# Performance work log

Measured on AMD Instinct MI355X. Metric: run time of the kernel, lower is better.

## Reference

```python
import jax, jax.numpy as jnp
import numpy as np

K = 32
TEMP = 0.01
OTHERWEIGHT = 0.5
BS = 64
F = 128


def setup_inputs() -> dict:
    key = jax.random.key(0)
    k1, k2, k3 = jax.random.split(key, 3)
    feats1 = jax.random.normal(k1, (K * BS, F), dtype=jnp.float32)
    feats2 = jax.random.normal(k2, (K * BS, F), dtype=jnp.float32)
    overlap_inds = jax.random.randint(k3, (K,), 0, 2).astype(bool)
    return {"feats1": feats1, "feats2": feats2, "overlap_inds": overlap_inds, "bs": BS}


def _labels(overlap_inds, bs):
    k = overlap_inds.shape[0]
    labels1 = jnp.repeat(jnp.arange(k), bs)
    nov = (~overlap_inds).astype(jnp.int32)
    excl_nov = jnp.cumsum(nov) - nov  # exclusive count of non-overlaps before i
    class2 = jnp.where(overlap_inds, jnp.arange(k), k + excl_nov)
    labels2 = jnp.repeat(class2, bs)
    return jnp.concatenate([labels1, labels2])


def reference(feats1, feats2, overlap_inds, bs):
    n1 = feats1.shape[0]
    labels = _labels(overlap_inds, bs)            # [n]
    feats = jnp.concatenate([feats1, feats2])     # [n, F]
    n = feats.shape[0]

    logits = (feats @ feats.T) * TEMP             # [n, n]; log of exp(sim*temp)
    sim = jnp.exp(logits)

    same = labels[:, None] == labels[None, :]
    eye = jnp.eye(n, dtype=bool)
    pos_mask = same & ~eye
    neg_mask = ~same

    is2 = jnp.arange(n) >= n1                     # second-view block indicator
    cross_w = jnp.where(is2[:, None] != is2[None, :], OTHERWEIGHT, 1.0)

    neg_sum = jnp.sum(jnp.where(neg_mask, sim, 0.0), axis=1)      # [n]
    # -log(pos / neg_sum) = log(neg_sum) - logits
    per_pair_loss = cross_w * (jnp.log(neg_sum)[:, None] - logits)
    total_loss = jnp.sum(jnp.where(pos_mask, per_pair_loss, 0.0))
    total_pos = jnp.sum(pos_mask)

    # accuracy: a positive pair counts iff its sim beats ALL negatives in its row
    max_neg = jnp.max(jnp.where(neg_mask, sim, -jnp.inf), axis=1)  # [n]
    correct = pos_mask & (sim > max_neg[:, None])
    acc = jnp.sum(correct).astype(jnp.float32) / total_pos.astype(jnp.float32)

    loss = total_loss / total_pos.astype(jnp.float32)
    return acc, loss
```

## Files before the change

kernel.cpp:

```cpp
#include <hip/hip_runtime.h>
#include <math.h>

#define TEMP 0.01f

typedef __attribute__((ext_vector_type(8))) short short8;
typedef __attribute__((ext_vector_type(4))) float f32x4;
typedef __attribute__((ext_vector_type(8))) unsigned short ushort8_t;


__device__ __forceinline__ unsigned bf16_hi_bits(float x) {
  unsigned u = __float_as_uint(x);
  return (u + 0x7FFFu + ((u >> 16) & 1u)) >> 16;
}

struct HL { unsigned short h, l; };

__device__ __forceinline__ HL split1(float x) {
  unsigned hb = bf16_hi_bits(x);
  float hf = __uint_as_float(hb << 16);
  unsigned lb = bf16_hi_bits(x - hf);
  HL r;
  r.h = (unsigned short)hb;
  r.l = (unsigned short)lb;
  return r;
}

__device__ __forceinline__ void decode_ov(const int* __restrict__ ov_raw,
                                          int* s_class2, int* s_v2b,
                                          int* s_ov) {
  const int t = threadIdx.x;
  if (t < 64) {
    int v = (t < 32) ? ov_raw[t] : 0;
    bool valid = (t >= 32) || (v == 0) || (v == 1);
    unsigned long long okmask = __ballot(valid);
    bool as_int = (okmask == ~0ull);
    s_v2b[t] = 0;
    if (t < 32) {
      int o = as_int ? v : (((const unsigned char*)ov_raw)[t] ? 1 : 0);
      s_ov[t] = o;
      unsigned long long nz = __ballot((t < 32) && !o);
      int cum = __popcll(nz & ((1ull << t) - 1ull));
      int c2 = o ? t : 32 + cum;
      s_class2[t] = c2;
      s_v2b[c2] = t;
    }
  }
}

__device__ __forceinline__ int labf(int g, const int* s_class2) {
  return (g < 2048) ? (g >> 6) : s_class2[(g - 2048) >> 6];
}

__device__ __forceinline__ int slotf(int g, int cls, const int* s_v2b) {
  if (g < 2048) return g - (cls << 6);
  return ((cls < 32) ? 64 : 0) + (g - 2048 - (s_v2b[cls] << 6));
}

__global__ __launch_bounds__(256) void precompute_kernel(
    const float* __restrict__ f1, const float* __restrict__ f2,
    unsigned short* __restrict__ Ph, unsigned short* __restrict__ Pl) {
  const int u = blockIdx.x * 256 + threadIdx.x;
  const int row = u >> 4;
  const int gid = u & 15;
  const int kc = gid >> 3, P = gid & 7;
  const int k = kc * 64 + (P ^ (row & 7)) * 8;
  const float* src = (row < 2048) ? (f1 + (size_t)row * 128)
                                  : (f2 + (size_t)(row - 2048) * 128);
  const float4 a = *(const float4*)(src + k);
  const float4 b = *(const float4*)(src + k + 4);
  ushort8_t hi, lo;
  HL s;
  s = split1(a.x); hi.s0 = s.h; lo.s0 = s.l;
  s = split1(a.y); hi.s1 = s.h; lo.s1 = s.l;
  s = split1(a.z); hi.s2 = s.h; lo.s2 = s.l;
  s = split1(a.w); hi.s3 = s.h; lo.s3 = s.l;
  s = split1(b.x); hi.s4 = s.h; lo.s4 = s.l;
  s = split1(b.y); hi.s5 = s.h; lo.s5 = s.l;
  s = split1(b.z); hi.s6 = s.h; lo.s6 = s.l;
  s = split1(b.w); hi.s7 = s.h; lo.s7 = s.l;
  *(ushort8_t*)&Ph[(size_t)row * 128 + gid * 8] = hi;
  *(ushort8_t*)&Pl[(size_t)row * 128 + gid * 8] = lo;
}

__device__ __forceinline__ void compute_tile(
    int ibase, int jbase, bool diag,
    const unsigned short* __restrict__ Ph, const unsigned short* __restrict__ Pl,
    unsigned short (*Ah)[64], unsigned short (*Al)[64],
    unsigned short (*Bh)[64], unsigned short (*Bl)[64],
    const int* s_class2, const int* s_v2b,
    float* __restrict__ nsum, int* __restrict__ nmaxb,
    float* __restrict__ pcw, float* __restrict__ pcwl,
    float* __restrict__ posbuf) {
  const int t = threadIdx.x;
  const int l = t & 63;
  const int wid = t >> 6;
  const int wy = wid >> 1, wx = wid & 1;
  const int rr = l & 15;
  const int q = l >> 4;
  const int sw = l & 7;

  f32x4 acc[4][4];
#pragma unroll
  for (int mi = 0; mi < 4; ++mi)
#pragma unroll
    for (int ni = 0; ni < 4; ++ni) acc[mi][ni] = (f32x4)0.0f;

  const int gg = t & 7;
  const int r0 = t >> 3;

  for (int kc = 0; kc < 2; ++kc) {
    __syncthreads();
#pragma unroll
    for (int p = 0; p < 4; ++p) {
      const int r = r0 + 32 * p;
      const size_t arec = (size_t)(ibase + r) * 128 + kc * 64 + gg * 8;
      const ushort8_t vah = *(const ushort8_t*)&Ph[arec];
      const ushort8_t val = *(const ushort8_t*)&Pl[arec];
      *(ushort8_t*)&Ah[r][gg * 8] = vah;
      *(ushort8_t*)&Al[r][gg * 8] = val;
      if (!diag) {
        const size_t brec = (size_t)(jbase + r) * 128 + kc * 64 + gg * 8;
        const ushort8_t vbh = *(const ushort8_t*)&Ph[brec];
        const ushort8_t vbl = *(const ushort8_t*)&Pl[brec];
        *(ushort8_t*)&Bh[r][gg * 8] = vbh;
        *(ushort8_t*)&Bl[r][gg * 8] = vbl;
      }
    }
    __syncthreads();

#pragma unroll
    for (int s = 0; s < 2; ++s) {
      const int pb = ((((s << 2) | q)) ^ sw) << 3;
      short8 afh[4], afl[4], bfh[4], bfl[4];
#pragma unroll
      for (int mi = 0; mi < 4; ++mi) {
        const int ar = wy * 64 + mi * 16 + rr;
        afh[mi] = *(const short8*)&Ah[ar][pb];
        afl[mi] = *(const short8*)&Al[ar][pb];
        const int br = wx * 64 + mi * 16 + rr;
        bfh[mi] = diag ? *(const short8*)&Ah[br][pb]
                       : *(const short8*)&Bh[br][pb];
        bfl[mi] = diag ? *(const short8*)&Al[br][pb]
                       : *(const short8*)&Bl[br][pb];
      }
#pragma unroll
      for (int mi = 0; mi < 4; ++mi)
#pragma unroll
        for (int ni = 0; ni < 4; ++ni) {
          acc[mi][ni] = __builtin_amdgcn_mfma_f32_16x16x32_bf16(
              afh[mi], bfh[ni], acc[mi][ni], 0, 0, 0);
          acc[mi][ni] = __builtin_amdgcn_mfma_f32_16x16x32_bf16(
              afh[mi], bfl[ni], acc[mi][ni], 0, 0, 0);
          acc[mi][ni] = __builtin_amdgcn_mfma_f32_16x16x32_bf16(
              afl[mi], bfh[ni], acc[mi][ni], 0, 0, 0);
        }
    }
  }

  const bool off = !diag;
  const float cw = ((ibase < 2048) != (jbase < 2048)) ? 0.5f : 1.0f;
  int gj[4], lj[4];
#pragma unroll
  for (int ni = 0; ni < 4; ++ni) {
    gj[ni] = jbase + wx * 64 + ni * 16 + rr;
    lj[ni] = labf(gj[ni], s_class2);
  }

  float cnsum[4], cnmax[4], cpcw[4], cpcwl[4];
#pragma unroll
  for (int ni = 0; ni < 4; ++ni) {
    cnsum[ni] = 0.f; cnmax[ni] = 0.f; cpcw[ni] = 0.f; cpcwl[ni] = 0.f;
  }

#pragma unroll
  for (int mi = 0; mi < 4; ++mi) {
#pragma unroll
    for (int reg = 0; reg < 4; ++reg) {
      const int gi = ibase + wy * 64 + mi * 16 + q * 4 + reg;
      const int li = labf(gi, s_class2);
      float rnsum = 0.f, rnmax = 0.f, rpcw = 0.f, rpcwl = 0.f;
#pragma unroll
      for (int ni = 0; ni < 4; ++ni) {
        const int gjj = gj[ni];
        if (gi == gjj) continue;
        const float logit = acc[mi][ni][reg] * TEMP;
        const float e = __expf(logit);
        if (li == lj[ni]) {
          rpcw += cw;
          rpcwl += cw * logit;
          posbuf[(size_t)gi * 128 + slotf(gjj, li, s_v2b)] = e;
          if (off) {
            cpcw[ni] += cw;
            cpcwl[ni] += cw * logit;
            posbuf[(size_t)gjj * 128 + slotf(gi, li, s_v2b)] = e;
          }
        } else {
          rnsum += e;
          rnmax = fmaxf(rnmax, e);
          if (off) {
            cnsum[ni] += e;
            cnmax[ni] = fmaxf(cnmax[ni], e);
          }
        }
      }
#pragma unroll
      for (int m = 1; m < 16; m <<= 1) {
        rnsum += __shfl_xor(rnsum, m, 64);
        rpcw  += __shfl_xor(rpcw, m, 64);
        rpcwl += __shfl_xor(rpcwl, m, 64);
        rnmax = fmaxf(rnmax, __shfl_xor(rnmax, m, 64));
      }
      if (rr == 0) {
        atomicAdd(&nsum[gi], rnsum);
        atomicAdd(&pcw[gi], rpcw);
        atomicAdd(&pcwl[gi], rpcwl);
        atomicMax(&nmaxb[gi], __float_as_int(rnmax));
      }
    }
  }

  if (off) {
#pragma unroll
    for (int ni = 0; ni < 4; ++ni) {
      float cs = cnsum[ni], cm = cnmax[ni], cp = cpcw[ni], cl = cpcwl[ni];
#pragma unroll
      for (int m = 16; m < 64; m <<= 1) {
        cs += __shfl_xor(cs, m, 64);
        cp += __shfl_xor(cp, m, 64);
        cl += __shfl_xor(cl, m, 64);
        cm = fmaxf(cm, __shfl_xor(cm, m, 64));
      }
      if (q == 0) {
        const int g = gj[ni];
        atomicAdd(&nsum[g], cs);
        atomicAdd(&pcw[g], cp);
        atomicAdd(&pcwl[g], cl);
        atomicMax(&nmaxb[g], __float_as_int(cm));
      }
    }
  }
}

__global__ __launch_bounds__(256, 2) void main_kernel(
    const unsigned short* __restrict__ Ph, const unsigned short* __restrict__ Pl,
    const int* __restrict__ ov_raw, float* __restrict__ nsum,
    int* __restrict__ nmaxb, float* __restrict__ pcw,
    float* __restrict__ pcwl, float* __restrict__ posbuf) {
  __shared__ unsigned short Ah[128][64], Al[128][64];
  __shared__ unsigned short Bh[128][64], Bl[128][64];
  __shared__ int s_class2[32], s_v2b[64], s_ov[32];

  decode_ov(ov_raw, s_class2, s_v2b, s_ov);

  const int bid = blockIdx.x;
  if (bid < 496) {
    int idx = bid, bi = 0;
    while (idx >= 31 - bi) { idx -= 31 - bi; ++bi; }
    const int bj = bi + 1 + idx;
    compute_tile(bi * 128, bj * 128, false, Ph, Pl, Ah, Al, Bh, Bl, s_class2,
                 s_v2b, nsum, nmaxb, pcw, pcwl, posbuf);
  } else {
    const int d = (bid - 496) * 2;
    compute_tile(d * 128, d * 128, true, Ph, Pl, Ah, Al, Bh, Bl, s_class2,
                 s_v2b, nsum, nmaxb, pcw, pcwl, posbuf);
    compute_tile((d + 1) * 128, (d + 1) * 128, true, Ph, Pl, Ah, Al, Bh, Bl,
                 s_class2, s_v2b, nsum, nmaxb, pcw, pcwl, posbuf);
  }
}

__global__ __launch_bounds__(256) void finalize_kernel(
    const int* __restrict__ ov_raw, const float* __restrict__ nsum,
    const int* __restrict__ nmaxb, const float* __restrict__ pcw,
    const float* __restrict__ pcwl, const float* __restrict__ posbuf,
    float* __restrict__ accum, int* __restrict__ counter,
    float* __restrict__ out) {
  __shared__ int s_class2[32], s_v2b[64], s_ov[32];
  __shared__ float sc[4], sp[4], sl[4];
  decode_ov(ov_raw, s_class2, s_v2b, s_ov);
  __syncthreads();

  const int t = threadIdx.x;
  const int w = t >> 6, lane = t & 63;
  float cnt_acc = 0.f, pos_acc = 0.f, loss_acc = 0.f;
  const int rbase = blockIdx.x * 64 + w * 16;
  for (int i = 0; i < 16; ++i) {
    const int row = rbase + i;
    const float2 pv = *(const float2*)&posbuf[(size_t)row * 128 + lane * 2];
    const int c = labf(row, s_class2);
    const int size = (c < 32) ? (s_ov[c] ? 128 : 64) : 64;
    int selfslot;
    if (row < 2048) selfslot = row - (c << 6);
    else selfslot = ((c < 32) ? 64 : 0) + (row - 2048 - (s_v2b[c] << 6));
    const float nmax = __int_as_float(nmaxb[row]);
    const int s0 = lane * 2;
    int h = 0;
    if (s0 < size && s0 != selfslot && pv.x > nmax) h++;
    if (s0 + 1 < size && s0 + 1 != selfslot && pv.y > nmax) h++;
    cnt_acc += (float)h;
    if (lane == 0) {
      loss_acc += logf(nsum[row]) * pcw[row] - pcwl[row];
      pos_acc += (float)(size - 1);
    }
  }
#pragma unroll
  for (int m = 1; m < 64; m <<= 1) {
    cnt_acc += __shfl_xor(cnt_acc, m, 64);
    pos_acc += __shfl_xor(pos_acc, m, 64);
    loss_acc += __shfl_xor(loss_acc, m, 64);
  }
  if (lane == 0) { sc[w] = cnt_acc; sp[w] = pos_acc; sl[w] = loss_acc; }
  __syncthreads();
  if (t == 0) {
    atomicAdd(&accum[0], sc[0] + sc[1] + sc[2] + sc[3]);
    atomicAdd(&accum[1], sp[0] + sp[1] + sp[2] + sp[3]);
    atomicAdd(&accum[2], sl[0] + sl[1] + sl[2] + sl[3]);
    __threadfence();
    const int prev = atomicAdd(counter, 1);
    if (prev == 63) {
      const float c = atomicAdd(&accum[0], 0.0f);
      const float tp = atomicAdd(&accum[1], 0.0f);
      const float lo = atomicAdd(&accum[2], 0.0f);
      out[0] = c / tp;
      out[1] = lo / tp;
    }
  }
}

extern "C" void kernel_launch(void* const* d_in, const int* in_sizes, int n_in,
                              void* d_out, int out_size, void* d_ws,
                              size_t ws_size, hipStream_t stream) {
  const float* f1 = (const float*)d_in[0];
  const float* f2 = (const float*)d_in[1];
  const int* ov = (const int*)d_in[2];
  float* out = (float*)d_out;

  float* wsf = (float*)d_ws;
  int* wsi = (int*)d_ws;
  float* nsum   = wsf;
  int* nmaxb    = wsi + 4096;
  float* pcw    = wsf + 8192;
  float* pcwl   = wsf + 12288;
  float* accum  = wsf + 16384;
  int* counter  = wsi + 16387;
  float* posbuf = wsf + 16400;
  unsigned short* Ph = (unsigned short*)(wsf + 540688);
  unsigned short* Pl = Ph + 524288;

  (void)hipMemsetAsync(nsum, 0, (size_t)16392 * sizeof(float), stream);

  precompute_kernel<<<256, 256, 0, stream>>>(f1, f2, Ph, Pl);
  main_kernel<<<512, 256, 0, stream>>>(Ph, Pl, ov, nsum, nmaxb, pcw, pcwl,
                                       posbuf);
  finalize_kernel<<<64, 256, 0, stream>>>(ov, nsum, nmaxb, pcw, pcwl, posbuf,
                                          accum, counter, out);
}
```

Measured before the change: 111.4 us.

## Load MFMA fragments directly from global memory, dropping LDS staging

The main kernel no longer stages the bf16 hi/lo tiles through shared memory. Each wave now reads its MFMA operand fragments straight from global memory (relying on L2/L1), and the precompute kernel drops its XOR swizzle layout to match. Without the LDS buffers, launch bounds are raised to 4 blocks per CU, and the grid becomes one tile per block over the upper triangle including diagonals (528 blocks). This removes the LDS copies and the syncthreads barriers, in exchange for redundant global and cache traffic and exposed load latency.

Measured after the change: 123.5 us. 1.11x slower.

```diff
diff --git a/kernel.cpp b/kernel.cpp
--- a/kernel.cpp
+++ b/kernel.cpp
@@ -61,9 +61,8 @@
     unsigned short* __restrict__ Ph, unsigned short* __restrict__ Pl) {
   const int u = blockIdx.x * 256 + threadIdx.x;
   const int row = u >> 4;
-  const int gid = u & 15;
-  const int kc = gid >> 3, P = gid & 7;
-  const int k = kc * 64 + (P ^ (row & 7)) * 8;
+  const int seg = u & 15;
+  const int k = seg * 8;
   const float* src = (row < 2048) ? (f1 + (size_t)row * 128)
                                   : (f2 + (size_t)(row - 2048) * 128);
   const float4 a = *(const float4*)(src + k);
@@ -78,26 +77,37 @@
   s = split1(b.y); hi.s5 = s.h; lo.s5 = s.l;
   s = split1(b.z); hi.s6 = s.h; lo.s6 = s.l;
   s = split1(b.w); hi.s7 = s.h; lo.s7 = s.l;
-  *(ushort8_t*)&Ph[(size_t)row * 128 + gid * 8] = hi;
-  *(ushort8_t*)&Pl[(size_t)row * 128 + gid * 8] = lo;
-}
-
-__device__ __forceinline__ void compute_tile(
-    int ibase, int jbase, bool diag,
+  *(ushort8_t*)&Ph[(size_t)row * 128 + k] = hi;
+  *(ushort8_t*)&Pl[(size_t)row * 128 + k] = lo;
+}
+
+__global__ __launch_bounds__(256, 4) void main_kernel(
     const unsigned short* __restrict__ Ph, const unsigned short* __restrict__ Pl,
-    unsigned short (*Ah)[64], unsigned short (*Al)[64],
-    unsigned short (*Bh)[64], unsigned short (*Bl)[64],
-    const int* s_class2, const int* s_v2b,
-    float* __restrict__ nsum, int* __restrict__ nmaxb,
-    float* __restrict__ pcw, float* __restrict__ pcwl,
-    float* __restrict__ posbuf) {
+    const int* __restrict__ ov_raw, float* __restrict__ nsum,
+    int* __restrict__ nmaxb, float* __restrict__ pcw,
+    float* __restrict__ pcwl, float* __restrict__ posbuf) {
+  __shared__ int s_class2[32], s_v2b[64], s_ov[32];
+
+  decode_ov(ov_raw, s_class2, s_v2b, s_ov);
+  __syncthreads();
+
+  int idx = blockIdx.x, bi = 0;
+  while (idx >= 32 - bi) { idx -= 32 - bi; ++bi; }
+  const int bj = bi + idx;
+  const bool diag = (bi == bj);
+  const int ibase = bi * 128, jbase = bj * 128;
+
   const int t = threadIdx.x;
   const int l = t & 63;
   const int wid = t >> 6;
   const int wy = wid >> 1, wx = wid & 1;
   const int rr = l & 15;
   const int q = l >> 4;
-  const int sw = l & 7;
+
+  const unsigned short* PA = Ph + ((size_t)(ibase + wy * 64 + rr) << 7) + q * 8;
+  const unsigned short* LA = Pl + ((size_t)(ibase + wy * 64 + rr) << 7) + q * 8;
+  const unsigned short* PB = Ph + ((size_t)(jbase + wx * 64 + rr) << 7) + q * 8;
+  const unsigned short* LB = Pl + ((size_t)(jbase + wx * 64 + rr) << 7) + q * 8;
 
   f32x4 acc[4][4];
 #pragma unroll
@@ -105,55 +115,28 @@
 #pragma unroll
     for (int ni = 0; ni < 4; ++ni) acc[mi][ni] = (f32x4)0.0f;
 
-  const int gg = t & 7;
-  const int r0 = t >> 3;
-
-  for (int kc = 0; kc < 2; ++kc) {
-    __syncthreads();
-#pragma unroll
-    for (int p = 0; p < 4; ++p) {
-      const int r = r0 + 32 * p;
-      const size_t arec = (size_t)(ibase + r) * 128 + kc * 64 + gg * 8;
-      const ushort8_t vah = *(const ushort8_t*)&Ph[arec];
-      const ushort8_t val = *(const ushort8_t*)&Pl[arec];
-      *(ushort8_t*)&Ah[r][gg * 8] = vah;
-      *(ushort8_t*)&Al[r][gg * 8] = val;
-      if (!diag) {
-        const size_t brec = (size_t)(jbase + r) * 128 + kc * 64 + gg * 8;
-        const ushort8_t vbh = *(const ushort8_t*)&Ph[brec];
-        const ushort8_t vbl = *(const ushort8_t*)&Pl[brec];
-        *(ushort8_t*)&Bh[r][gg * 8] = vbh;
-        *(ushort8_t*)&Bl[r][gg * 8] = vbl;
-      }
-    }
-    __syncthreads();
-
-#pragma unroll
-    for (int s = 0; s < 2; ++s) {
-      const int pb = ((((s << 2) | q)) ^ sw) << 3;
-      short8 afh[4], afl[4], bfh[4], bfl[4];
-#pragma unroll
-      for (int mi = 0; mi < 4; ++mi) {
-        const int ar = wy * 64 + mi * 16 + rr;
-        afh[mi] = *(const short8*)&Ah[ar][pb];
-        afl[mi] = *(const short8*)&Al[ar][pb];
-        const int br = wx * 64 + mi * 16 + rr;
-        bfh[mi] = diag ? *(const short8*)&Ah[br][pb]
-                       : *(const short8*)&Bh[br][pb];
-        bfl[mi] = diag ? *(const short8*)&Al[br][pb]
-                       : *(const short8*)&Bl[br][pb];
-      }
-#pragma unroll
-      for (int mi = 0; mi < 4; ++mi)
-#pragma unroll
-        for (int ni = 0; ni < 4; ++ni) {
-          acc[mi][ni] = __builtin_amdgcn_mfma_f32_16x16x32_bf16(
-              afh[mi], bfh[ni], acc[mi][ni], 0, 0, 0);
-          acc[mi][ni] = __builtin_amdgcn_mfma_f32_16x16x32_bf16(
-              afh[mi], bfl[ni], acc[mi][ni], 0, 0, 0);
-          acc[mi][ni] = __builtin_amdgcn_mfma_f32_16x16x32_bf16(
-              afl[mi], bfh[ni], acc[mi][ni], 0, 0, 0);
-        }
+#pragma unroll
+  for (int ks = 0; ks < 4; ++ks) {
+    const int ko = ks * 32;
+    short8 bfh[4], bfl[4];
+#pragma unroll
+    for (int ni = 0; ni < 4; ++ni) {
+      bfh[ni] = *(const short8*)(PB + ni * 2048 + ko);
+      bfl[ni] = *(const short8*)(LB + ni * 2048 + ko);
+    }
+#pragma unroll
+    for (int mi = 0; mi < 4; ++mi) {
+      const short8 afh = *(const short8*)(PA + mi * 2048 + ko);
+      const short8 afl = *(const short8*)(LA + mi * 2048 + ko);
+#pragma unroll
+      for (int ni = 0; ni < 4; ++ni) {
+        acc[mi][ni] = __builtin_amdgcn_mfma_f32_16x16x32_bf16(
+            afh, bfh[ni], acc[mi][ni], 0, 0, 0);
+        acc[mi][ni] = __builtin_amdgcn_mfma_f32_16x16x32_bf16(
+            afh, bfl[ni], acc[mi][ni], 0, 0, 0);
+        acc[mi][ni] = __builtin_amdgcn_mfma_f32_16x16x32_bf16(
+            afl, bfh[ni], acc[mi][ni], 0, 0, 0);
+      }
     }
   }
 
@@ -241,33 +224,6 @@
   }
 }
 
-__global__ __launch_bounds__(256, 2) void main_kernel(
-    const unsigned short* __restrict__ Ph, const unsigned short* __restrict__ Pl,
-    const int* __restrict__ ov_raw, float* __restrict__ nsum,
-    int* __restrict__ nmaxb, float* __restrict__ pcw,
-    float* __restrict__ pcwl, float* __restrict__ posbuf) {
-  __shared__ unsigned short Ah[128][64], Al[128][64];
-  __shared__ unsigned short Bh[128][64], Bl[128][64];
-  __shared__ int s_class2[32], s_v2b[64], s_ov[32];
-
-  decode_ov(ov_raw, s_class2, s_v2b, s_ov);
-
-  const int bid = blockIdx.x;
-  if (bid < 496) {
-    int idx = bid, bi = 0;
-    while (idx >= 31 - bi) { idx -= 31 - bi; ++bi; }
-    const int bj = bi + 1 + idx;
-    compute_tile(bi * 128, bj * 128, false, Ph, Pl, Ah, Al, Bh, Bl, s_class2,
-                 s_v2b, nsum, nmaxb, pcw, pcwl, posbuf);
-  } else {
-    const int d = (bid - 496) * 2;
-    compute_tile(d * 128, d * 128, true, Ph, Pl, Ah, Al, Bh, Bl, s_class2,
-                 s_v2b, nsum, nmaxb, pcw, pcwl, posbuf);
-    compute_tile((d + 1) * 128, (d + 1) * 128, true, Ph, Pl, Ah, Al, Bh, Bl,
-                 s_class2, s_v2b, nsum, nmaxb, pcw, pcwl, posbuf);
-  }
-}
-
 __global__ __launch_bounds__(256) void finalize_kernel(
     const int* __restrict__ ov_raw, const float* __restrict__ nsum,
     const int* __restrict__ nmaxb, const float* __restrict__ pcw,
@@ -349,7 +305,7 @@
   (void)hipMemsetAsync(nsum, 0, (size_t)16392 * sizeof(float), stream);
 
   precompute_kernel<<<256, 256, 0, stream>>>(f1, f2, Ph, Pl);
-  main_kernel<<<512, 256, 0, stream>>>(Ph, Pl, ov, nsum, nmaxb, pcw, pcwl,
+  main_kernel<<<528, 256, 0, stream>>>(Ph, Pl, ov, nsum, nmaxb, pcw, pcwl,
                                        posbuf);
   finalize_kernel<<<64, 256, 0, stream>>>(ov, nsum, nmaxb, pcw, pcwl, posbuf,
                                           accum, counter, out);
```

## Replace per-row global atomics with per-tile partial slots reduced in finalize

Applied to the files above, without the earlier changes.

Each tile now writes its per-row partial negative sum, weighted positive sums and negative max as one float4 into a dedicated slot (64 slots per row), instead of issuing four global atomics per row. The finalize kernel loads the 64 partials per row and reduces them with wave shuffles. This removes atomic contention and most of the memset, at the cost of a 4 MB partial buffer that has to be written and read back. Every slot must be written exactly once, and the layout appears to cover all 32 column tiles times 2 wave halves.

After: 112.1 us. About the same (+0.7%).

```diff
diff --git a/kernel.cpp b/kernel.cpp
--- a/kernel.cpp
+++ b/kernel.cpp
@@ -83,14 +83,13 @@
 }
 
 __device__ __forceinline__ void compute_tile(
-    int ibase, int jbase, bool diag,
+    int bi, int bj, bool diag,
     const unsigned short* __restrict__ Ph, const unsigned short* __restrict__ Pl,
     unsigned short (*Ah)[64], unsigned short (*Al)[64],
     unsigned short (*Bh)[64], unsigned short (*Bl)[64],
     const int* s_class2, const int* s_v2b,
-    float* __restrict__ nsum, int* __restrict__ nmaxb,
-    float* __restrict__ pcw, float* __restrict__ pcwl,
-    float* __restrict__ posbuf) {
+    float4* __restrict__ P4, float* __restrict__ posbuf) {
+  const int ibase = bi * 128, jbase = bj * 128;
   const int t = threadIdx.x;
   const int l = t & 63;
   const int wid = t >> 6;
@@ -211,10 +210,8 @@
         rnmax = fmaxf(rnmax, __shfl_xor(rnmax, m, 64));
       }
       if (rr == 0) {
-        atomicAdd(&nsum[gi], rnsum);
-        atomicAdd(&pcw[gi], rpcw);
-        atomicAdd(&pcwl[gi], rpcwl);
-        atomicMax(&nmaxb[gi], __float_as_int(rnmax));
+        float4 v; v.x = rnsum; v.y = rpcw; v.z = rpcwl; v.w = rnmax;
+        P4[(size_t)gi * 64 + (bj * 2 + wx)] = v;
       }
     }
   }
@@ -231,11 +228,8 @@
         cm = fmaxf(cm, __shfl_xor(cm, m, 64));
       }
       if (q == 0) {
-        const int g = gj[ni];
-        atomicAdd(&nsum[g], cs);
-        atomicAdd(&pcw[g], cp);
-        atomicAdd(&pcwl[g], cl);
-        atomicMax(&nmaxb[g], __float_as_int(cm));
+        float4 v; v.x = cs; v.y = cp; v.z = cl; v.w = cm;
+        P4[(size_t)gj[ni] * 64 + (bi * 2 + wy)] = v;
       }
     }
   }
@@ -243,9 +237,8 @@
 
 __global__ __launch_bounds__(256, 2) void main_kernel(
     const unsigned short* __restrict__ Ph, const unsigned short* __restrict__ Pl,
-    const int* __restrict__ ov_raw, float* __restrict__ nsum,
-    int* __restrict__ nmaxb, float* __restrict__ pcw,
-    float* __restrict__ pcwl, float* __restrict__ posbuf) {
+    const int* __restrict__ ov_raw, float4* __restrict__ P4,
+    float* __restrict__ posbuf) {
   __shared__ unsigned short Ah[128][64], Al[128][64];
   __shared__ unsigned short Bh[128][64], Bl[128][64];
   __shared__ int s_class2[32], s_v2b[64], s_ov[32];
@@ -257,23 +250,21 @@
     int idx = bid, bi = 0;
     while (idx >= 31 - bi) { idx -= 31 - bi; ++bi; }
     const int bj = bi + 1 + idx;
-    compute_tile(bi * 128, bj * 128, false, Ph, Pl, Ah, Al, Bh, Bl, s_class2,
-                 s_v2b, nsum, nmaxb, pcw, pcwl, posbuf);
+    compute_tile(bi, bj, false, Ph, Pl, Ah, Al, Bh, Bl, s_class2, s_v2b, P4,
+                 posbuf);
   } else {
     const int d = (bid - 496) * 2;
-    compute_tile(d * 128, d * 128, true, Ph, Pl, Ah, Al, Bh, Bl, s_class2,
-                 s_v2b, nsum, nmaxb, pcw, pcwl, posbuf);
-    compute_tile((d + 1) * 128, (d + 1) * 128, true, Ph, Pl, Ah, Al, Bh, Bl,
-                 s_class2, s_v2b, nsum, nmaxb, pcw, pcwl, posbuf);
+    compute_tile(d, d, true, Ph, Pl, Ah, Al, Bh, Bl, s_class2, s_v2b, P4,
+                 posbuf);
+    compute_tile(d + 1, d + 1, true, Ph, Pl, Ah, Al, Bh, Bl, s_class2, s_v2b,
+                 P4, posbuf);
   }
 }
 
 __global__ __launch_bounds__(256) void finalize_kernel(
-    const int* __restrict__ ov_raw, const float* __restrict__ nsum,
-    const int* __restrict__ nmaxb, const float* __restrict__ pcw,
-    const float* __restrict__ pcwl, const float* __restrict__ posbuf,
-    float* __restrict__ accum, int* __restrict__ counter,
-    float* __restrict__ out) {
+    const int* __restrict__ ov_raw, const float4* __restrict__ P4,
+    const float* __restrict__ posbuf, float* __restrict__ accum,
+    int* __restrict__ counter, float* __restrict__ out) {
   __shared__ int s_class2[32], s_v2b[64], s_ov[32];
   __shared__ float sc[4], sp[4], sl[4];
   decode_ov(ov_raw, s_class2, s_v2b, s_ov);
@@ -285,20 +276,28 @@
   const int rbase = blockIdx.x * 64 + w * 16;
   for (int i = 0; i < 16; ++i) {
     const int row = rbase + i;
+    float4 p = P4[(size_t)row * 64 + lane];
+#pragma unroll
+    for (int m = 1; m < 64; m <<= 1) {
+      p.x += __shfl_xor(p.x, m, 64);
+      p.y += __shfl_xor(p.y, m, 64);
+      p.z += __shfl_xor(p.z, m, 64);
+      p.w = fmaxf(p.w, __shfl_xor(p.w, m, 64));
+    }
+    const float nmax = p.w;
     const float2 pv = *(const float2*)&posbuf[(size_t)row * 128 + lane * 2];
     const int c = labf(row, s_class2);
     const int size = (c < 32) ? (s_ov[c] ? 128 : 64) : 64;
     int selfslot;
     if (row < 2048) selfslot = row - (c << 6);
     else selfslot = ((c < 32) ? 64 : 0) + (row - 2048 - (s_v2b[c] << 6));
-    const float nmax = __int_as_float(nmaxb[row]);
     const int s0 = lane * 2;
     int h = 0;
     if (s0 < size && s0 != selfslot && pv.x > nmax) h++;
     if (s0 + 1 < size && s0 + 1 != selfslot && pv.y > nmax) h++;
     cnt_acc += (float)h;
     if (lane == 0) {
-      loss_acc += logf(nsum[row]) * pcw[row] - pcwl[row];
+      loss_acc += logf(p.x) * p.y - p.z;
       pos_acc += (float)(size - 1);
     }
   }
@@ -336,21 +335,16 @@
 
   float* wsf = (float*)d_ws;
   int* wsi = (int*)d_ws;
-  float* nsum   = wsf;
-  int* nmaxb    = wsi + 4096;
-  float* pcw    = wsf + 8192;
-  float* pcwl   = wsf + 12288;
-  float* accum  = wsf + 16384;
-  int* counter  = wsi + 16387;
-  float* posbuf = wsf + 16400;
-  unsigned short* Ph = (unsigned short*)(wsf + 540688);
+  float* accum  = wsf;
+  int* counter  = wsi + 3;
+  float* posbuf = wsf + 16;
+  float4* P4    = (float4*)(wsf + 524304);
+  unsigned short* Ph = (unsigned short*)(wsf + 1572880);
   unsigned short* Pl = Ph + 524288;
 
-  (void)hipMemsetAsync(nsum, 0, (size_t)16392 * sizeof(float), stream);
+  (void)hipMemsetAsync(accum, 0, 16, stream);
 
   precompute_kernel<<<256, 256, 0, stream>>>(f1, f2, Ph, Pl);
-  main_kernel<<<512, 256, 0, stream>>>(Ph, Pl, ov, nsum, nmaxb, pcw, pcwl,
-                                       posbuf);
-  finalize_kernel<<<64, 256, 0, stream>>>(ov, nsum, nmaxb, pcw, pcwl, posbuf,
-                                          accum, counter, out);
-}
+  main_kernel<<<512, 256, 0, stream>>>(Ph, Pl, ov, P4, posbuf);
+  finalize_kernel<<<64, 256, 0, stream>>>(ov, P4, posbuf, accum, counter, out);
+}
```
